# Kernel tuning notes

Hardware: AMD Instinct MI355X
Metric: run time of the kernel (lower is better)

## Reference

```python
import jax, jax.numpy as jnp
import numpy as np

N = 100000   # nodes
E = 6400000  # edges (avg degree 64)
F = 512      # num_features
C = 16       # num_classes

def _glorot(key, shape):
    fan_in, fan_out = shape
    lim = (6.0 / (fan_in + fan_out)) ** 0.5
    return jax.random.uniform(key, shape, jnp.float32, -lim, lim)

def setup_inputs() -> dict:
    key = jax.random.key(0)
    ks = jax.random.split(key, 8)
    x = jax.random.normal(ks[0], (N, F), jnp.float32)
    edge_index = jax.random.randint(ks[1], (2, E), 0, N, dtype=jnp.int64)
    return {
        "x": x,
        "edge_index": edge_index,
        "W1": _glorot(ks[2], (F, 16)), "b1": jnp.zeros((16,), jnp.float32),
        "W2": _glorot(ks[3], (16, 32)), "b2": jnp.zeros((32,), jnp.float32),
        "W3": _glorot(ks[4], (32, C)),  "b3": jnp.zeros((C,), jnp.float32),
        "Wc": _glorot(ks[5], (C, C)),   "bc": jnp.zeros((C,), jnp.float32),
    }

def _gcn_conv(x, row, col, norm, W, b):
    # PyG GCNConv: transform, then normalized sum-aggregation, then bias
    h = x @ W                                   # [N, out]
    msg = h[row] * norm[:, None]                # gather + scale, [E+N, out]
    agg = jax.ops.segment_sum(msg, col, num_segments=N)
    return agg + b

def reference(x, edge_index, W1, b1, W2, b2, W3, b3, Wc, bc):
    n = x.shape[0]
    loops = jnp.arange(n, dtype=edge_index.dtype)
    row = jnp.concatenate([edge_index[0], loops])  # source
    col = jnp.concatenate([edge_index[1], loops])  # target
    # symmetric normalization D^{-1/2} A_hat D^{-1/2}
    deg = jax.ops.segment_sum(jnp.ones_like(col, dtype=x.dtype), col, num_segments=n)
    dis = jnp.where(deg > 0, jax.lax.rsqrt(deg), 0.0)
    norm = dis[row] * dis[col]                     # [E+N]
    h = jax.nn.relu(_gcn_conv(x, row, col, norm, W1, b1))
    h = jax.nn.relu(_gcn_conv(h, row, col, norm, W2, b2))
    h = jax.nn.relu(_gcn_conv(h, row, col, norm, W3, b3))
    out = h @ Wc + bc
    return (out, h)
```

## Files before the change

### kernel.cpp

```cpp
#include <hip/hip_runtime.h>
#include <hip/hip_bf16.h>
#include <hip/hip_fp16.h>
#include <stdint.h>


__device__ __forceinline__ int blockScanExclusive256(int v, int* wsum) {
  int lane = threadIdx.x & 63;
  int wid  = threadIdx.x >> 6;
  int inc = v;
#pragma unroll
  for (int d = 1; d < 64; d <<= 1) {
    int y = __shfl_up(inc, d, 64);
    if (lane >= d) inc += y;
  }
  if (lane == 63) wsum[wid] = inc;
  __syncthreads();
  if (threadIdx.x == 0) {
    int s = 0;
#pragma unroll
    for (int w = 0; w < 4; ++w) { int t = wsum[w]; wsum[w] = s; s += t; }
  }
  __syncthreads();
  return inc - v + wsum[wid];
}

__device__ __forceinline__ int blockScanExclusive512(int v, int* wsum) {
  int lane = threadIdx.x & 63;
  int wid  = threadIdx.x >> 6;
  int inc = v;
#pragma unroll
  for (int d = 1; d < 64; d <<= 1) {
    int y = __shfl_up(inc, d, 64);
    if (lane >= d) inc += y;
  }
  if (lane == 63) wsum[wid] = inc;
  __syncthreads();
  if (threadIdx.x == 0) {
    int s = 0;
#pragma unroll
    for (int w = 0; w < 8; ++w) { int t = wsum[w]; wsum[w] = s; s += t; }
  }
  __syncthreads();
  return inc - v + wsum[wid];
}

__global__ __launch_bounds__(256) void k_bhist(const int* __restrict__ ecol,
                                               int* __restrict__ cntmat,
                                               int e, int chunk, int nb) {
  __shared__ int h[256];
  h[threadIdx.x] = 0;
  __syncthreads();
  int g = blockIdx.x;
  int s0 = g * chunk;
  int s1 = min(e, s0 + chunk);
  int i = s0 + threadIdx.x;
  for (; i + 768 < s1; i += 1024) {
    int c0 = ecol[i], c1 = ecol[i + 256], c2 = ecol[i + 512], c3 = ecol[i + 768];
    atomicAdd(&h[c0 >> 9], 1);
    atomicAdd(&h[c1 >> 9], 1);
    atomicAdd(&h[c2 >> 9], 1);
    atomicAdd(&h[c3 >> 9], 1);
  }
  for (; i < s1; i += 256) atomicAdd(&h[ecol[i] >> 9], 1);
  __syncthreads();
  for (int b = threadIdx.x; b < nb; b += 256) cntmat[g * nb + b] = h[b];
}

__global__ __launch_bounds__(256) void k_colscan(int* __restrict__ cntmat,
                                                 int* __restrict__ colsum,
                                                 int G, int nb) {
  __shared__ int wsum[4];
  __shared__ int carry_s;
  int b = blockIdx.x;
  if (threadIdx.x == 0) carry_s = 0;
  __syncthreads();
  for (int base = 0; base < G; base += 256) {
    int i = base + threadIdx.x;
    int v = (i < G) ? cntmat[i * nb + b] : 0;
    int ex = blockScanExclusive256(v, wsum);
    int c = carry_s;
    __syncthreads();
    if (i < G) cntmat[i * nb + b] = ex + c;
    if (threadIdx.x == 255) carry_s = c + ex + v;
    __syncthreads();
  }
  if (threadIdx.x == 0) colsum[b] = carry_s;
}

__global__ __launch_bounds__(256) void k_bscan(const int* __restrict__ colsum,
                                               int* __restrict__ bbase,
                                               int nb, int etot) {
  __shared__ int wsum[4];
  __shared__ int carry_s;
  if (threadIdx.x == 0) carry_s = 0;
  __syncthreads();
  for (int base = 0; base < nb; base += 256) {
    int i = base + threadIdx.x;
    int v = (i < nb) ? colsum[i] : 0;
    int ex = blockScanExclusive256(v, wsum);
    int c = carry_s;
    __syncthreads();
    if (i < nb) bbase[i] = ex + c;
    if (threadIdx.x == 255) carry_s = c + ex + v;
    __syncthreads();
  }
  if (threadIdx.x == 0) bbase[nb] = etot;
}

__global__ __launch_bounds__(256) void k_scat_xf(
    const int* __restrict__ erow, const int* __restrict__ ecol,
    const int* __restrict__ cntmat, const int* __restrict__ bbase,
    unsigned* __restrict__ sorted, int e, int chunk, int nb, int gs,
    const float* __restrict__ x, const float* __restrict__ W,
    __half* __restrict__ t1raw, int n) {
  if ((int)blockIdx.x < gs) {
    __shared__ int base[256];
    int g = blockIdx.x;
    for (int b = threadIdx.x; b < nb; b += 256)
      base[b] = bbase[b] + cntmat[g * nb + b];
    __syncthreads();
    int s0 = g * chunk;
    int s1 = min(e, s0 + chunk);
    int i = s0 + threadIdx.x;
    for (; i + 768 < s1; i += 1024) {
      int c0 = ecol[i],       c1 = ecol[i + 256], c2 = ecol[i + 512], c3 = ecol[i + 768];
      int r0 = erow[i],       r1 = erow[i + 256], r2 = erow[i + 512], r3 = erow[i + 768];
      int p0 = atomicAdd(&base[c0 >> 9], 1);
      int p1 = atomicAdd(&base[c1 >> 9], 1);
      int p2 = atomicAdd(&base[c2 >> 9], 1);
      int p3 = atomicAdd(&base[c3 >> 9], 1);
      sorted[p0] = ((unsigned)r0 << 9) | (unsigned)(c0 & 511);
      sorted[p1] = ((unsigned)r1 << 9) | (unsigned)(c1 & 511);
      sorted[p2] = ((unsigned)r2 << 9) | (unsigned)(c2 & 511);
      sorted[p3] = ((unsigned)r3 << 9) | (unsigned)(c3 & 511);
    }
    for (; i < s1; i += 256) {
      int c = ecol[i];
      int p = atomicAdd(&base[c >> 9], 1);
      sorted[p] = ((unsigned)erow[i] << 9) | (unsigned)(c & 511);
    }
    return;
  }

  int L = threadIdx.x & 63;
  int wid = (blockIdx.x - gs) * 4 + (threadIdx.x >> 6);
  int nw = (gridDim.x - gs) * 4;

  float w[8][16];
  const float4* W4 = reinterpret_cast<const float4*>(W);
#pragma unroll
  for (int i = 0; i < 4; ++i) {
#pragma unroll
    for (int c4 = 0; c4 < 4; ++c4) {
      float4 va = W4[(4 * L + i) * 4 + c4];
      w[i][c4 * 4 + 0] = va.x; w[i][c4 * 4 + 1] = va.y;
      w[i][c4 * 4 + 2] = va.z; w[i][c4 * 4 + 3] = va.w;
      float4 vb = W4[(256 + 4 * L + i) * 4 + c4];
      w[4 + i][c4 * 4 + 0] = vb.x; w[4 + i][c4 * 4 + 1] = vb.y;
      w[4 + i][c4 * 4 + 2] = vb.z; w[4 + i][c4 * 4 + 3] = vb.w;
    }
  }
  int col = ((L & 1) << 3) | ((L & 2) << 1) | ((L & 4) >> 1) | ((L & 8) >> 3);

  for (int r = wid; r < n; r += nw) {
    const float4* xr = reinterpret_cast<const float4*>(x + (size_t)r * 512);
    float4 v0 = xr[L];
    float4 v1 = xr[64 + L];
    float acc[16];
#pragma unroll
    for (int c = 0; c < 16; ++c) {
      float a = v0.x * w[0][c];
      a = fmaf(v0.y, w[1][c], a);
      a = fmaf(v0.z, w[2][c], a);
      a = fmaf(v0.w, w[3][c], a);
      a = fmaf(v1.x, w[4][c], a);
      a = fmaf(v1.y, w[5][c], a);
      a = fmaf(v1.z, w[6][c], a);
      a = fmaf(v1.w, w[7][c], a);
      acc[c] = a;
    }
#pragma unroll
    for (int j = 0; j < 8; ++j) {
      float send = (L & 1) ? acc[j] : acc[j + 8];
      float recv = __shfl_xor(send, 1, 64);
      acc[j] = ((L & 1) ? acc[j + 8] : acc[j]) + recv;
    }
#pragma unroll
    for (int j = 0; j < 4; ++j) {
      float send = (L & 2) ? acc[j] : acc[j + 4];
      float recv = __shfl_xor(send, 2, 64);
      acc[j] = ((L & 2) ? acc[j + 4] : acc[j]) + recv;
    }
#pragma unroll
    for (int j = 0; j < 2; ++j) {
      float send = (L & 4) ? acc[j] : acc[j + 2];
      float recv = __shfl_xor(send, 4, 64);
      acc[j] = ((L & 4) ? acc[j + 2] : acc[j]) + recv;
    }
    {
      float send = (L & 8) ? acc[0] : acc[1];
      float recv = __shfl_xor(send, 8, 64);
      acc[0] = ((L & 8) ? acc[1] : acc[0]) + recv;
    }
    float s = acc[0];
    s += __shfl_xor(s, 16, 64);
    s += __shfl_xor(s, 32, 64);
    if (L < 16) t1raw[r * 16 + col] = __float2half(s);
  }
}

__global__ __launch_bounds__(512) void k_pass2(const unsigned* __restrict__ sorted,
                                               const int* __restrict__ bbase,
                                               float* __restrict__ dis,
                                               int* __restrict__ rowptr,
                                               __half* __restrict__ t1,
                                               int* __restrict__ csr,
                                               int n, int etot) {
  __shared__ int hist[512];
  __shared__ int cur[512];
  __shared__ int wsum[8];
  int b = blockIdx.x;
  hist[threadIdx.x] = 0;
  __syncthreads();
  int s0 = bbase[b], s1 = bbase[b + 1];
  for (int i = s0 + threadIdx.x; i < s1; i += 512)
    atomicAdd(&hist[sorted[i] & 511], 1);
  __syncthreads();
  int j = threadIdx.x;
  int node = (b << 9) + j;
  int deg = hist[j];
  int ex = blockScanExclusive512(deg, wsum);
  float dv = rsqrtf((float)(deg + 1));
  cur[j] = s0 + ex;
  if (node < n) {
    dis[node] = dv;
    rowptr[node] = s0 + ex;
    __half2* t2 = reinterpret_cast<__half2*>(t1 + ((size_t)node << 4));
#pragma unroll
    for (int q = 0; q < 8; ++q) {
      float2 fv = __half22float2(t2[q]);
      fv.x *= dv; fv.y *= dv;
      t2[q] = __float22half2_rn(fv);
    }
  }
  if (b == 0 && threadIdx.x == 0) rowptr[n] = etot;
  __syncthreads();
  for (int i = s0 + threadIdx.x; i < s1; i += 512) {
    unsigned v = sorted[i];
    int pos = atomicAdd(&cur[v & 511], 1);
    csr[pos] = (int)(v >> 9);
  }
}

__device__ __forceinline__ float gather16(const __half* __restrict__ hs,
                                          const int* __restrict__ rowptr,
                                          const int* __restrict__ csr,
                                          int node, int f) {
  float acc0 = __half2float(hs[(node << 4) + f]);
  int e0 = rowptr[node], e1 = rowptr[node + 1];
  int e = e0;
  float acc1 = 0.f, acc2 = 0.f, acc3 = 0.f;
  for (; e + 16 <= e1; e += 16) {
    int r0  = csr[e + 0],  r1  = csr[e + 1],  r2  = csr[e + 2],  r3  = csr[e + 3];
    int r4  = csr[e + 4],  r5  = csr[e + 5],  r6  = csr[e + 6],  r7  = csr[e + 7];
    int r8  = csr[e + 8],  r9  = csr[e + 9],  r10 = csr[e + 10], r11 = csr[e + 11];
    int r12 = csr[e + 12], r13 = csr[e + 13], r14 = csr[e + 14], r15 = csr[e + 15];
    __half v0  = hs[(r0  << 4) + f], v1  = hs[(r1  << 4) + f];
    __half v2  = hs[(r2  << 4) + f], v3  = hs[(r3  << 4) + f];
    __half v4  = hs[(r4  << 4) + f], v5  = hs[(r5  << 4) + f];
    __half v6  = hs[(r6  << 4) + f], v7  = hs[(r7  << 4) + f];
    __half v8  = hs[(r8  << 4) + f], v9  = hs[(r9  << 4) + f];
    __half v10 = hs[(r10 << 4) + f], v11 = hs[(r11 << 4) + f];
    __half v12 = hs[(r12 << 4) + f], v13 = hs[(r13 << 4) + f];
    __half v14 = hs[(r14 << 4) + f], v15 = hs[(r15 << 4) + f];
    acc0 += (__half2float(v0)  + __half2float(v1))  + (__half2float(v2)  + __half2float(v3));
    acc1 += (__half2float(v4)  + __half2float(v5))  + (__half2float(v6)  + __half2float(v7));
    acc2 += (__half2float(v8)  + __half2float(v9))  + (__half2float(v10) + __half2float(v11));
    acc3 += (__half2float(v12) + __half2float(v13)) + (__half2float(v14) + __half2float(v15));
  }
  for (; e + 4 <= e1; e += 4) {
    int r0 = csr[e + 0], r1 = csr[e + 1], r2 = csr[e + 2], r3 = csr[e + 3];
    float v0 = __half2float(hs[(r0 << 4) + f]), v1 = __half2float(hs[(r1 << 4) + f]);
    float v2 = __half2float(hs[(r2 << 4) + f]), v3 = __half2float(hs[(r3 << 4) + f]);
    acc0 += (v0 + v1) + (v2 + v3);
  }
  for (; e < e1; ++e) acc0 += __half2float(hs[(csr[e] << 4) + f]);
  return (acc0 + acc1) + (acc2 + acc3);
}

__global__ __launch_bounds__(256) void k_agg_rb(
    const __half* __restrict__ hs, const int* __restrict__ rowptr,
    const int* __restrict__ csr, const float* __restrict__ dis,
    const float* __restrict__ b, __half* __restrict__ out, int n) {
  int node = blockIdx.x * 16 + threadIdx.x / 16;
  int f = threadIdx.x % 16;
  if (node >= n) return;
  float acc = gather16(hs, rowptr, csr, node, f);
  float d = dis[node];
  float t = fmaxf(fmaf(d, acc, b[f]), 0.f);
  out[(node << 4) + f] = __float2half(t * d);
}

__global__ __launch_bounds__(256) void k_agg_mid(
    const __half* __restrict__ hs, const int* __restrict__ rowptr,
    const int* __restrict__ csr, const float* __restrict__ dis,
    const float* __restrict__ W2, const float* __restrict__ b2,
    const float* __restrict__ W3, __half* __restrict__ out, int n) {
  __shared__ float w2s[512];
  __shared__ float w3s[512];
  __shared__ float b2s[32];
  for (int i = threadIdx.x; i < 512; i += 256) { w2s[i] = W2[i]; w3s[i] = W3[i]; }
  if (threadIdx.x < 32) b2s[threadIdx.x] = b2[threadIdx.x];
  __syncthreads();
  int node = blockIdx.x * 16 + threadIdx.x / 16;
  int f = threadIdx.x % 16;
  if (node >= n) return;
  float acc = gather16(hs, rowptr, csr, node, f);
  float d = dis[node];
  float v = d * acc;
  int base = threadIdx.x & 48;
  float a0 = b2s[f], a1 = b2s[f + 16];
#pragma unroll
  for (int k = 0; k < 16; ++k) {
    float vk = __shfl(v, base + k, 64);
    a0 = fmaf(vk, w2s[k * 32 + f], a0);
    a1 = fmaf(vk, w2s[k * 32 + 16 + f], a1);
  }
  a0 = fmaxf(a0, 0.f);
  a1 = fmaxf(a1, 0.f);
  float t = 0.f;
#pragma unroll
  for (int c = 0; c < 16; ++c) {
    float h0 = __shfl(a0, base + c, 64);
    float h1 = __shfl(a1, base + c, 64);
    t = fmaf(h0, w3s[c * 16 + f], t);
    t = fmaf(h1, w3s[(c + 16) * 16 + f], t);
  }
  out[(node << 4) + f] = __float2half(t * d);
}

__global__ __launch_bounds__(256) void k_agg_out(
    const __half* __restrict__ hs, const int* __restrict__ rowptr,
    const int* __restrict__ csr, const float* __restrict__ dis,
    const float* __restrict__ b3, const float* __restrict__ Wc,
    const float* __restrict__ bc, float* __restrict__ outh,
    float* __restrict__ outc, int n) {
  __shared__ float wcs[256];
  __shared__ float b3s[16];
  __shared__ float bcs[16];
  if (threadIdx.x < 256) wcs[threadIdx.x] = Wc[threadIdx.x];
  if (threadIdx.x < 16) { b3s[threadIdx.x] = b3[threadIdx.x]; bcs[threadIdx.x] = bc[threadIdx.x]; }
  __syncthreads();
  int node = blockIdx.x * 16 + threadIdx.x / 16;
  int f = threadIdx.x % 16;
  if (node >= n) return;
  float acc = gather16(hs, rowptr, csr, node, f);
  float d = dis[node];
  float h = fmaxf(fmaf(d, acc, b3s[f]), 0.f);
  outh[(node << 4) + f] = h;
  int base = threadIdx.x & 48;
  float o = bcs[f];
#pragma unroll
  for (int k = 0; k < 16; ++k) {
    float hk = __shfl(h, base + k, 64);
    o = fmaf(hk, wcs[k * 16 + f], o);
  }
  outc[(node << 4) + f] = o;
}

extern "C" void kernel_launch(void* const* d_in, const int* in_sizes, int n_in,
                              void* d_out, int out_size, void* d_ws, size_t ws_size,
                              hipStream_t stream) {
  (void)n_in; (void)out_size;
  const float* x  = (const float*)d_in[0];
  const int*   ei = (const int*)d_in[1];
  const float* W1 = (const float*)d_in[2];
  const float* b1 = (const float*)d_in[3];
  const float* W2 = (const float*)d_in[4];
  const float* b2 = (const float*)d_in[5];
  const float* W3 = (const float*)d_in[6];
  const float* b3 = (const float*)d_in[7];
  const float* Wc = (const float*)d_in[8];
  const float* bc = (const float*)d_in[9];

  const int F = 512;
  int N = in_sizes[0] / F;
  int E = in_sizes[1] / 2;
  const int* erow = ei;
  const int* ecol = ei + E;
  int NB = (N + 511) >> 9;
  const int GS = 512;
  const int GT = 1536;
  int chunk = (E + GS - 1) / GS;

  auto align = [](size_t v) { return (v + 255) & ~(size_t)255; };
  char* p = (char*)d_ws;
  int*   cntmat = (int*)p;   p += align((size_t)GS * NB * 4);
  int*   colsum = (int*)p;   p += align(256 * 4);
  int*   bbase  = (int*)p;   p += align(257 * 4);
  float* dis    = (float*)p; p += align((size_t)N * 4);
  int*   rowptr = (int*)p;   p += align(((size_t)N + 1) * 4);
  int*   csr    = (int*)p;   p += align((size_t)E * 4);
  unsigned* sorted = (unsigned*)p; p += align((size_t)E * 4);
  __half* bufA = (__half*)p; p += align((size_t)N * 16 * 2);
  __half* bufB = (__half*)p; p += align((size_t)N * 16 * 2);
  if ((size_t)(p - (char*)d_ws) > ws_size) return;

  float* outc = (float*)d_out;
  float* outh = (float*)d_out + (size_t)N * 16;

  k_bhist<<<GS, 256, 0, stream>>>(ecol, cntmat, E, chunk, NB);
  k_colscan<<<NB, 256, 0, stream>>>(cntmat, colsum, GS, NB);
  k_bscan<<<1, 256, 0, stream>>>(colsum, bbase, NB, E);
  k_scat_xf<<<GS + GT, 256, 0, stream>>>(erow, ecol, cntmat, bbase, sorted, E,
                                         chunk, NB, GS, x, W1, bufA, N);
  k_pass2<<<NB, 512, 0, stream>>>(sorted, bbase, dis, rowptr, bufA, csr, N, E);

  k_agg_rb<<<(N + 15) / 16, 256, 0, stream>>>(bufA, rowptr, csr, dis, b1, bufB, N);
  k_agg_mid<<<(N + 15) / 16, 256, 0, stream>>>(bufB, rowptr, csr, dis, W2, b2, W3, bufA, N);
  k_agg_out<<<(N + 15) / 16, 256, 0, stream>>>(bufA, rowptr, csr, dis, b3, Wc, bc, outh, outc, N);
}
```

Baseline: 318.5 us.

## Stage bucket scatter in LDS for coalesced writes, split transform kernel

The edge bucket scatter now stages each block's chunk in shared memory, grouped by bucket with a local scan, then writes each bucket's run to global memory contiguously. The aim is to replace scattered 4-byte global stores with coalesced ones. The chunk size is fixed at 15360 edges, so the grid grows to about 417 blocks. Each block uses roughly 60KB of LDS, which limits occupancy. The fused scatter plus x@W1 kernel is split into two launches, which gives up the overlap between the two.

```diff
diff --git a/kernel.cpp b/kernel.cpp
--- a/kernel.cpp
+++ b/kernel.cpp
@@ -3,6 +3,8 @@
 #include <hip/hip_fp16.h>
 #include <stdint.h>
 
+
+#define MS_CHUNK 15360
 
 __device__ __forceinline__ int blockScanExclusive256(int v, int* wsum) {
   int lane = threadIdx.x & 63;
@@ -107,44 +109,68 @@
   if (threadIdx.x == 0) bbase[nb] = etot;
 }
 
-__global__ __launch_bounds__(256) void k_scat_xf(
+__global__ __launch_bounds__(256) void k_scatter_ms(
     const int* __restrict__ erow, const int* __restrict__ ecol,
-    const int* __restrict__ cntmat, const int* __restrict__ bbase,
-    unsigned* __restrict__ sorted, int e, int chunk, int nb, int gs,
+    const int* __restrict__ cntmat, const int* __restrict__ colsum,
+    const int* __restrict__ bbase, unsigned* __restrict__ sorted,
+    int e, int chunk, int nb, int G) {
+  __shared__ unsigned staging[MS_CHUNK];
+  __shared__ int lstart[256];
+  __shared__ int lfill[256];
+  __shared__ int gbase[256];
+  __shared__ int wsum[4];
+  int g = blockIdx.x;
+  for (int b = threadIdx.x; b < nb; b += 256) {
+    int cur = cntmat[g * nb + b];
+    int nxt = (g + 1 < G) ? cntmat[(g + 1) * nb + b] : colsum[b];
+    lfill[b] = nxt - cur;
+    gbase[b] = bbase[b] + cur;
+  }
+  __syncthreads();
+  int v = (threadIdx.x < nb) ? lfill[threadIdx.x] : 0;
+  int ex = blockScanExclusive256(v, wsum);
+  if (threadIdx.x < nb) lstart[threadIdx.x] = ex;
+  __syncthreads();
+  if (threadIdx.x < nb) lfill[threadIdx.x] = 0;
+  __syncthreads();
+  int s0 = g * chunk;
+  int s1 = min(e, s0 + chunk);
+  int i = s0 + threadIdx.x;
+  for (; i + 768 < s1; i += 1024) {
+    int c0 = ecol[i],       c1 = ecol[i + 256], c2 = ecol[i + 512], c3 = ecol[i + 768];
+    int r0 = erow[i],       r1 = erow[i + 256], r2 = erow[i + 512], r3 = erow[i + 768];
+    int b0 = c0 >> 9, b1 = c1 >> 9, b2 = c2 >> 9, b3 = c3 >> 9;
+    int p0 = atomicAdd(&lfill[b0], 1);
+    int p1 = atomicAdd(&lfill[b1], 1);
+    int p2 = atomicAdd(&lfill[b2], 1);
+    int p3 = atomicAdd(&lfill[b3], 1);
+    staging[lstart[b0] + p0] = ((unsigned)r0 << 9) | (unsigned)(c0 & 511);
+    staging[lstart[b1] + p1] = ((unsigned)r1 << 9) | (unsigned)(c1 & 511);
+    staging[lstart[b2] + p2] = ((unsigned)r2 << 9) | (unsigned)(c2 & 511);
+    staging[lstart[b3] + p3] = ((unsigned)r3 << 9) | (unsigned)(c3 & 511);
+  }
+  for (; i < s1; i += 256) {
+    int c = ecol[i];
+    int b = c >> 9;
+    int p = atomicAdd(&lfill[b], 1);
+    staging[lstart[b] + p] = ((unsigned)erow[i] << 9) | (unsigned)(c & 511);
+  }
+  __syncthreads();
+  int wid = threadIdx.x >> 6, L = threadIdx.x & 63;
+  for (int b = wid; b < nb; b += 4) {
+    int len = lfill[b];
+    int ls = lstart[b], gb = gbase[b];
+    for (int j = L; j < len; j += 64)
+      sorted[gb + j] = staging[ls + j];
+  }
+}
+
+__global__ __launch_bounds__(256) void k_transform1(
     const float* __restrict__ x, const float* __restrict__ W,
     __half* __restrict__ t1raw, int n) {
-  if ((int)blockIdx.x < gs) {
-    __shared__ int base[256];
-    int g = blockIdx.x;
-    for (int b = threadIdx.x; b < nb; b += 256)
-      base[b] = bbase[b] + cntmat[g * nb + b];
-    __syncthreads();
-    int s0 = g * chunk;
-    int s1 = min(e, s0 + chunk);
-    int i = s0 + threadIdx.x;
-    for (; i + 768 < s1; i += 1024) {
-      int c0 = ecol[i],       c1 = ecol[i + 256], c2 = ecol[i + 512], c3 = ecol[i + 768];
-      int r0 = erow[i],       r1 = erow[i + 256], r2 = erow[i + 512], r3 = erow[i + 768];
-      int p0 = atomicAdd(&base[c0 >> 9], 1);
-      int p1 = atomicAdd(&base[c1 >> 9], 1);
-      int p2 = atomicAdd(&base[c2 >> 9], 1);
-      int p3 = atomicAdd(&base[c3 >> 9], 1);
-      sorted[p0] = ((unsigned)r0 << 9) | (unsigned)(c0 & 511);
-      sorted[p1] = ((unsigned)r1 << 9) | (unsigned)(c1 & 511);
-      sorted[p2] = ((unsigned)r2 << 9) | (unsigned)(c2 & 511);
-      sorted[p3] = ((unsigned)r3 << 9) | (unsigned)(c3 & 511);
-    }
-    for (; i < s1; i += 256) {
-      int c = ecol[i];
-      int p = atomicAdd(&base[c >> 9], 1);
-      sorted[p] = ((unsigned)erow[i] << 9) | (unsigned)(c & 511);
-    }
-    return;
-  }
-
   int L = threadIdx.x & 63;
-  int wid = (blockIdx.x - gs) * 4 + (threadIdx.x >> 6);
-  int nw = (gridDim.x - gs) * 4;
+  int wid = blockIdx.x * 4 + (threadIdx.x >> 6);
+  int nw = gridDim.x * 4;
 
   float w[8][16];
   const float4* W4 = reinterpret_cast<const float4*>(W);
@@ -389,9 +415,8 @@
   const int* erow = ei;
   const int* ecol = ei + E;
   int NB = (N + 511) >> 9;
-  const int GS = 512;
-  const int GT = 1536;
-  int chunk = (E + GS - 1) / GS;
+  const int chunk = MS_CHUNK;
+  int GS = (E + chunk - 1) / chunk;
 
   auto align = [](size_t v) { return (v + 255) & ~(size_t)255; };
   char* p = (char*)d_ws;
@@ -412,8 +437,9 @@
   k_bhist<<<GS, 256, 0, stream>>>(ecol, cntmat, E, chunk, NB);
   k_colscan<<<NB, 256, 0, stream>>>(cntmat, colsum, GS, NB);
   k_bscan<<<1, 256, 0, stream>>>(colsum, bbase, NB, E);
-  k_scat_xf<<<GS + GT, 256, 0, stream>>>(erow, ecol, cntmat, bbase, sorted, E,
-                                         chunk, NB, GS, x, W1, bufA, N);
+  k_scatter_ms<<<GS, 256, 0, stream>>>(erow, ecol, cntmat, colsum, bbase,
+                                       sorted, E, chunk, NB, GS);
+  k_transform1<<<2048, 256, 0, stream>>>(x, W1, bufA, N);
   k_pass2<<<NB, 512, 0, stream>>>(sorted, bbase, dis, rowptr, bufA, csr, N, E);
 
   k_agg_rb<<<(N + 15) / 16, 256, 0, stream>>>(bufA, rowptr, csr, dis, b1, bufB, N);
```

Measured after the change: 311.8 us. -2.1%, faster.
